# Optimization experiments

Hardware: AMD Instinct MI355X
Metric: run time of the kernel (lower is better)

Reference implementation:

```python
import jax, jax.numpy as jnp
import numpy as np

E = 1024   # embed_size
H = 16     # num_heads
D = E // H # head_dim
B, S = 4, 2048

def setup_inputs() -> dict:
    key = jax.random.key(0)
    ks = jax.random.split(key, 11)
    scale = 1.0 / np.sqrt(E)
    inp = {
        "Q": jax.random.normal(ks[0], (B, S, E), jnp.float32),
        "K": jax.random.normal(ks[1], (B, S, E), jnp.float32),
        "V": jax.random.normal(ks[2], (B, S, E), jnp.float32),
        "Wq": jax.random.uniform(ks[3], (E, E), jnp.float32, -scale, scale),
        "bq": jax.random.uniform(ks[4], (E,), jnp.float32, -scale, scale),
        "Wk": jax.random.uniform(ks[5], (E, E), jnp.float32, -scale, scale),
        "bk": jax.random.uniform(ks[6], (E,), jnp.float32, -scale, scale),
        "Wv": jax.random.uniform(ks[7], (E, E), jnp.float32, -scale, scale),
        "bv": jax.random.uniform(ks[8], (E,), jnp.float32, -scale, scale),
        "Wo": jax.random.uniform(ks[9], (E, E), jnp.float32, -scale, scale),
        "bo": jax.random.uniform(ks[10], (E,), jnp.float32, -scale, scale),
    }
    return inp

def reference(Q, K, V, Wq, bq, Wk, bk, Wv, bv, Wo, bo):
    b, sq, _ = Q.shape
    sk = K.shape[1]
    # Linear projections (torch Linear: x @ W.T + b), split into heads -> (b, H, s, D)
    q = (Q @ Wq.T + bq).reshape(b, sq, H, D).transpose(0, 2, 1, 3)
    k = (K @ Wk.T + bk).reshape(b, sk, H, D).transpose(0, 2, 1, 3)
    v = (V @ Wv.T + bv).reshape(b, sk, H, D).transpose(0, 2, 1, 3)
    scores = jnp.einsum('bhqd,bhkd->bhqk', q, k) / jnp.sqrt(jnp.float32(D))
    attn = jax.nn.softmax(scores, axis=-1)
    out = jnp.einsum('bhqk,bhkd->bhqd', attn, v)  # (b, H, sq, D)
    concat = out.transpose(0, 2, 1, 3).reshape(b, sq, E)
    return concat @ Wo.T + bo
```

## Files before the change

### kernel.cpp

```cpp
#include <hip/hip_runtime.h>
#include <hip/hip_bf16.h>

typedef unsigned short u16;
typedef unsigned int u32;
typedef __bf16 bf16x8 __attribute__((ext_vector_type(8)));
typedef float f32x4 __attribute__((ext_vector_type(4)));
typedef float f32x16 __attribute__((ext_vector_type(16)));
typedef unsigned int u32x2 __attribute__((ext_vector_type(2)));

constexpr int E_ = 1024, H_ = 16, D_ = 64, B_ = 4, S_ = 2048;
constexpr int GM = B_ * S_;
constexpr int GN = E_;
constexpr int GK = E_;

__device__ __forceinline__ u16 f2bf(float f) {
  union { float f; u32 u; } v; v.f = f;
  u32 r = v.u + 0x7fffu + ((v.u >> 16) & 1u);
  return (u16)(r >> 16);
}

__device__ __forceinline__ bf16x8 ld_bf16x8(const u16* p) {
  return *reinterpret_cast<const bf16x8*>(p);
}

__device__ __forceinline__ f32x4 mfma16(bf16x8 a, bf16x8 b, f32x4 c) {
  return __builtin_amdgcn_mfma_f32_16x16x32_bf16(a, b, c, 0, 0, 0);
}
__device__ __forceinline__ f32x16 mfma32(bf16x8 a, bf16x8 b, f32x16 c) {
  return __builtin_amdgcn_mfma_f32_32x32x16_bf16(a, b, c, 0, 0, 0);
}

__device__ __forceinline__ u32 cvtpk(float lo, float hi) {
  u32 r;
  asm("v_cvt_pk_bf16_f32 %0, %1, %2" : "=v"(r) : "v"(lo), "v"(hi));
  return r;
}

__device__ __forceinline__ void pl32swap(u32& a, u32& b) {
#if __has_builtin(__builtin_amdgcn_permlane32_swap)
  u32x2 r = __builtin_amdgcn_permlane32_swap(a, b, false, false);
  a = r.x; b = r.y;
#else
  asm volatile("v_permlane32_swap_b32 %0, %1" : "+v"(a), "+v"(b));
#endif
}

__device__ __forceinline__ float fexp2(float x) {
#if __has_builtin(__builtin_amdgcn_exp2f)
  return __builtin_amdgcn_exp2f(x);
#else
  return exp2f(x);
#endif
}

#define GLOAD_LDS16(gp, lp)                                                       \
  __builtin_amdgcn_global_load_lds(                                               \
      (const __attribute__((address_space(1))) u32*)(const void*)(gp),            \
      (__attribute__((address_space(3))) u32*)(void*)(lp), 16, 0, 0)

__global__ __launch_bounds__(256) void cvt7(
    const float4* __restrict__ s0, const float4* __restrict__ s1,
    const float4* __restrict__ s2, const float4* __restrict__ s3,
    const float4* __restrict__ s4, const float4* __restrict__ s5,
    const float4* __restrict__ s6,
    ushort4* __restrict__ d0, ushort4* __restrict__ d1,
    ushort4* __restrict__ d2, ushort4* __restrict__ d3,
    ushort4* __restrict__ d4, ushort4* __restrict__ d5,
    ushort4* __restrict__ d6) {
  long i = (long)blockIdx.x * 256 + threadIdx.x;
  const float4* s; ushort4* d; long j;
  if (i < 2097152L)      { s = s0; d = d0; j = i; }
  else if (i < 4194304L) { s = s1; d = d1; j = i - 2097152L; }
  else if (i < 6291456L) { s = s2; d = d2; j = i - 4194304L; }
  else if (i < 6553600L) { s = s3; d = d3; j = i - 6291456L; }
  else if (i < 6815744L) { s = s4; d = d4; j = i - 6553600L; }
  else if (i < 7077888L) { s = s5; d = d5; j = i - 6815744L; }
  else                   { s = s6; d = d6; j = i - 7077888L; }
  float4 v = s[j];
  ushort4 o;
  o.x = f2bf(v.x); o.y = f2bf(v.y); o.z = f2bf(v.z); o.w = f2bf(v.w);
  d[j] = o;
}

template <int MODE>
__global__ __launch_bounds__(256, 2) void gemm_bt(
    const u16* __restrict__ A, const u16* __restrict__ Bw,
    const float* __restrict__ bias, void* __restrict__ Cout, float scale) {
  __shared__ u16 As[128 * 32];
  __shared__ u16 Bs[128 * 32];
  const int tid = threadIdx.x;
  const int lane = tid & 63, w = tid >> 6;
  const int lr = lane & 15, lg = lane >> 4;
  const int bid = blockIdx.x;
  const int flat = (bid & 7) * 64 + (bid >> 3);
  const int bm = flat >> 3, bn = flat & 7;
  const int wm = (w >> 1) * 64, wn = (w & 1) * 64;

  f32x4 acc[4][4] = {};

  const int byte0 = (w * 2 + 0) * 1024 + lane * 16;
  const int byte1 = (w * 2 + 1) * 1024 + lane * 16;
  const int r0 = byte0 >> 6, c0 = (byte0 & 63) >> 1;
  const int r1 = byte1 >> 6, c1 = (byte1 & 63) >> 1;
  const u16* Arow0 = A + (size_t)(bm * 128 + r0) * GK + c0;
  const u16* Arow1 = A + (size_t)(bm * 128 + r1) * GK + c1;
  const u16* Brow0 = Bw + (size_t)(bn * 128 + r0) * GK + c0;
  const u16* Brow1 = Bw + (size_t)(bn * 128 + r1) * GK + c1;
  u16* As0 = &As[(w * 2 + 0) * 512];
  u16* As1 = &As[(w * 2 + 1) * 512];
  u16* Bs0 = &Bs[(w * 2 + 0) * 512];
  u16* Bs1 = &Bs[(w * 2 + 1) * 512];

  for (int kt = 0; kt < GK / 32; ++kt) {
    const int ko = kt * 32;
    GLOAD_LDS16(Arow0 + ko, As0);
    GLOAD_LDS16(Arow1 + ko, As1);
    GLOAD_LDS16(Brow0 + ko, Bs0);
    GLOAD_LDS16(Brow1 + ko, Bs1);
    __syncthreads();
    bf16x8 af[4], bf_[4];
#pragma unroll
    for (int mi = 0; mi < 4; ++mi)
      af[mi] = ld_bf16x8(&As[(wm + mi * 16 + lr) * 32 + lg * 8]);
#pragma unroll
    for (int ni = 0; ni < 4; ++ni)
      bf_[ni] = ld_bf16x8(&Bs[(wn + ni * 16 + lr) * 32 + lg * 8]);
#pragma unroll
    for (int mi = 0; mi < 4; ++mi)
#pragma unroll
      for (int ni = 0; ni < 4; ++ni)
        acc[mi][ni] = mfma16(af[mi], bf_[ni], acc[mi][ni]);
    __syncthreads();
  }

#pragma unroll
  for (int mi = 0; mi < 4; ++mi)
#pragma unroll
    for (int ni = 0; ni < 4; ++ni) {
      const int n = bn * 128 + wn + ni * 16 + lr;
      const float bv = bias[n];
#pragma unroll
      for (int r = 0; r < 4; ++r) {
        const int m = bm * 128 + wm + mi * 16 + lg * 4 + r;
        const float vv = (acc[mi][ni][r] + bv) * scale;
        if (MODE == 0) {
          const int b = m >> 11, s = m & 2047, h = n >> 6, d = n & 63;
          ((u16*)Cout)[(((size_t)(b * 16 + h) * 2048 + s) * 64) + d] = f2bf(vv);
        } else if (MODE == 1) {
          const int b = m >> 11, s = m & 2047, h = n >> 6, d = n & 63;
          ((u16*)Cout)[((size_t)(b * 16 + h) * 64 + d) * 2048 + s] = f2bf(vv);
        } else {
          ((float*)Cout)[(size_t)m * 1024 + n] = vv;
        }
      }
    }
}

__global__ __launch_bounds__(256, 2) void attn5(
    const u16* __restrict__ q, const u16* __restrict__ k,
    const u16* __restrict__ vT, u16* __restrict__ concat) {
  __shared__ u16 KT[2][64 * 64];
  __shared__ u16 VTl[2][64 * 64];
  const int tid = threadIdx.x, lane = tid & 63, w = tid >> 6;
  const int l31 = lane & 31, hi = lane >> 5;
  const int bid = blockIdx.x;
  const int flat = (bid & 7) * 64 + (bid >> 3);
  const int bh = flat >> 3, qt = flat & 7;
  const u16* qbp = q + (size_t)bh * S_ * D_;
  const char* kbase = (const char*)(k + (size_t)bh * S_ * D_);
  const char* vbase = (const char*)(vT + (size_t)bh * D_ * S_);
  const int q0 = qt * 256 + w * 64;

  bf16x8 qf[2][4];
#pragma unroll
  for (int qs = 0; qs < 2; ++qs)
#pragma unroll
    for (int kc = 0; kc < 4; ++kc)
      qf[qs][kc] =
          ld_bf16x8(&qbp[(size_t)(q0 + qs * 32 + l31) * 64 + kc * 16 + hi * 8]);

  f32x16 acc[2][2] = {};
  float l_[2] = {0.f, 0.f};

  const int srow = w * 8 + (lane >> 3);
  const int cswz = (((lane & 7) ^ (lane >> 3)) << 4);
  const char* gk0 = kbase + (size_t)srow * 128 + cswz;
  const char* gk1 = kbase + (size_t)(32 + srow) * 128 + cswz;
  const char* gv0 = vbase + (size_t)srow * (S_ * 2) + cswz;
  const char* gv1 = vbase + (size_t)(32 + srow) * (S_ * 2) + cswz;

  int col4[4];
#pragma unroll
  for (int c = 0; c < 4; ++c)
    col4[c] = (((c * 32 + hi * 16) ^ ((lane & 7) << 4)) >> 1);
  const int rrow = l31 * 64;

#define STAGE(t, buf)                                                     \
  do {                                                                    \
    GLOAD_LDS16(gk0 + (size_t)(t) * 8192, &KT[buf][(0 * 4 + w) * 512]);   \
    GLOAD_LDS16(gk1 + (size_t)(t) * 8192, &KT[buf][(1 * 4 + w) * 512]);   \
    GLOAD_LDS16(gv0 + (size_t)(t) * 128, &VTl[buf][(0 * 4 + w) * 512]);   \
    GLOAD_LDS16(gv1 + (size_t)(t) * 128, &VTl[buf][(1 * 4 + w) * 512]);   \
  } while (0)

  STAGE(0, 0);
  asm volatile("s_waitcnt vmcnt(0)" ::: "memory");
  __syncthreads();

  for (int t = 0; t < S_ / 64; ++t) {
    const int cur = t & 1, nxt = cur ^ 1;
    if (t < S_ / 64 - 1) STAGE(t + 1, nxt);

    f32x16 sF[2][2] = {};
#pragma unroll
    for (int st = 0; st < 2; ++st)
#pragma unroll
      for (int kc = 0; kc < 4; ++kc) {
        bf16x8 kf = ld_bf16x8(&KT[cur][st * 2048 + rrow + col4[kc]]);
        sF[0][st] = mfma32(kf, qf[0][kc], sF[0][st]);
        sF[1][st] = mfma32(kf, qf[1][kc], sF[1][st]);
      }

    bf16x8 vt[2][4];
#pragma unroll
    for (int ks = 0; ks < 4; ++ks) {
      vt[0][ks] = ld_bf16x8(&VTl[cur][rrow + col4[ks]]);
      vt[1][ks] = ld_bf16x8(&VTl[cur][2048 + rrow + col4[ks]]);
    }

#pragma unroll
    for (int qs = 0; qs < 2; ++qs) {
      float s0 = 0.f, s1 = 0.f, s2 = 0.f, s3 = 0.f;
#pragma unroll
      for (int st = 0; st < 2; ++st)
#pragma unroll
        for (int e = 0; e < 16; e += 4) {
          const float p0 = fexp2(sF[qs][st][e + 0]);
          const float p1 = fexp2(sF[qs][st][e + 1]);
          const float p2 = fexp2(sF[qs][st][e + 2]);
          const float p3 = fexp2(sF[qs][st][e + 3]);
          sF[qs][st][e + 0] = p0; sF[qs][st][e + 1] = p1;
          sF[qs][st][e + 2] = p2; sF[qs][st][e + 3] = p3;
          s0 += p0; s1 += p1; s2 += p2; s3 += p3;
        }
      l_[qs] += (s0 + s1) + (s2 + s3);

#pragma unroll
      for (int ks = 0; ks < 4; ++ks) {
        const int st = ks >> 1, b = (ks & 1) * 8;
        u32 w0 = cvtpk(sF[qs][st][b + 0], sF[qs][st][b + 1]);
        u32 w1 = cvtpk(sF[qs][st][b + 2], sF[qs][st][b + 3]);
        u32 w2 = cvtpk(sF[qs][st][b + 4], sF[qs][st][b + 5]);
        u32 w3 = cvtpk(sF[qs][st][b + 6], sF[qs][st][b + 7]);
        pl32swap(w0, w2);
        pl32swap(w1, w3);
        union { u32 u[4]; bf16x8 v; } pa;
        pa.u[0] = w0; pa.u[1] = w1; pa.u[2] = w2; pa.u[3] = w3;
        acc[qs][0] = mfma32(vt[0][ks], pa.v, acc[qs][0]);
        acc[qs][1] = mfma32(vt[1][ks], pa.v, acc[qs][1]);
      }
    }

    asm volatile("s_waitcnt vmcnt(0)" ::: "memory");
    __syncthreads();
  }
#undef STAGE

  const int b = bh >> 4, h = bh & 15;
#pragma unroll
  for (int qs = 0; qs < 2; ++qs) {
    u32 la = __builtin_bit_cast(u32, l_[qs]), lb = la;
    pl32swap(la, lb);
    const float lt =
        __builtin_bit_cast(float, la) + __builtin_bit_cast(float, lb);
    const float inv = 1.f / lt;
    const int s = q0 + qs * 32 + l31;
    u16* crow = concat + ((size_t)(b * 2048 + s)) * 1024 + h * 64;
#pragma unroll
    for (int dt = 0; dt < 2; ++dt)
#pragma unroll
      for (int g = 0; g < 4; ++g) {
        ushort4 o;
        o.x = f2bf(acc[qs][dt][g * 4 + 0] * inv);
        o.y = f2bf(acc[qs][dt][g * 4 + 1] * inv);
        o.z = f2bf(acc[qs][dt][g * 4 + 2] * inv);
        o.w = f2bf(acc[qs][dt][g * 4 + 3] * inv);
        *(ushort4*)&crow[dt * 32 + g * 8 + hi * 4] = o;
      }
  }
}

extern "C" void kernel_launch(void* const* d_in, const int* in_sizes, int n_in,
                              void* d_out, int out_size, void* d_ws,
                              size_t ws_size, hipStream_t stream) {
  const float* Qf = (const float*)d_in[0];
  const float* Kf = (const float*)d_in[1];
  const float* Vf = (const float*)d_in[2];
  const float* Wq = (const float*)d_in[3];
  const float* bq = (const float*)d_in[4];
  const float* Wk = (const float*)d_in[5];
  const float* bk = (const float*)d_in[6];
  const float* Wv = (const float*)d_in[7];
  const float* bv = (const float*)d_in[8];
  const float* Wo = (const float*)d_in[9];
  const float* bo = (const float*)d_in[10];

  char* ws = (char*)d_ws;
  u16* Xq = (u16*)(ws);
  u16* Xk = Xq + 8388608;
  u16* Xv = Xk + 8388608;
  u16* Wqb = (u16*)(ws + (size_t)3 * 16777216);
  u16* Wkb = Wqb + 1048576;
  u16* Wvb = Wkb + 1048576;
  u16* Wob = Wvb + 1048576;
  u16* qb = (u16*)(ws + (size_t)3 * 16777216 + 8388608);
  u16* kb = qb + (size_t)GM * GN;
  u16* vTb = kb + (size_t)GM * GN;
  u16* concat = Xq;

  cvt7<<<28672, 256, 0, stream>>>(
      (const float4*)Qf, (const float4*)Kf, (const float4*)Vf,
      (const float4*)Wq, (const float4*)Wk, (const float4*)Wv,
      (const float4*)Wo, (ushort4*)Xq, (ushort4*)Xk, (ushort4*)Xv,
      (ushort4*)Wqb, (ushort4*)Wkb, (ushort4*)Wvb, (ushort4*)Wob);

  gemm_bt<0><<<512, 256, 0, stream>>>(Xq, Wqb, bq, qb, 0.18033688011112042f);
  gemm_bt<0><<<512, 256, 0, stream>>>(Xk, Wkb, bk, kb, 1.0f);
  gemm_bt<1><<<512, 256, 0, stream>>>(Xv, Wvb, bv, vTb, 1.0f);

  attn5<<<512, 256, 0, stream>>>(qb, kb, vTb, concat);

  gemm_bt<2><<<512, 256, 0, stream>>>(concat, Wob, bo, (void*)d_out, 1.0f);
}
```

Baseline: 209.8 us.

## Split attention KV range across two blocks and merge partial outputs

```diff
diff --git a/kernel.cpp b/kernel.cpp
--- a/kernel.cpp
+++ b/kernel.cpp
@@ -156,20 +156,23 @@
     }
 }
 
-__global__ __launch_bounds__(256, 2) void attn5(
+__global__ __launch_bounds__(256, 2) void attn_part(
     const u16* __restrict__ q, const u16* __restrict__ k,
-    const u16* __restrict__ vT, u16* __restrict__ concat) {
+    const u16* __restrict__ vT, float* __restrict__ Ppart,
+    float* __restrict__ lpart) {
   __shared__ u16 KT[2][64 * 64];
   __shared__ u16 VTl[2][64 * 64];
   const int tid = threadIdx.x, lane = tid & 63, w = tid >> 6;
   const int l31 = lane & 31, hi = lane >> 5;
   const int bid = blockIdx.x;
-  const int flat = (bid & 7) * 64 + (bid >> 3);
-  const int bh = flat >> 3, qt = flat & 7;
+  const int flat = (bid & 7) * 128 + (bid >> 3);
+  const int gq = flat >> 1, half = flat & 1;
+  const int bh = gq >> 3, qt = gq & 7;
   const u16* qbp = q + (size_t)bh * S_ * D_;
   const char* kbase = (const char*)(k + (size_t)bh * S_ * D_);
   const char* vbase = (const char*)(vT + (size_t)bh * D_ * S_);
   const int q0 = qt * 256 + w * 64;
+  const int t0 = half * 16;
 
   bf16x8 qf[2][4];
 #pragma unroll
@@ -203,13 +206,13 @@
     GLOAD_LDS16(gv1 + (size_t)(t) * 128, &VTl[buf][(1 * 4 + w) * 512]);   \
   } while (0)
 
-  STAGE(0, 0);
+  STAGE(t0, 0);
   asm volatile("s_waitcnt vmcnt(0)" ::: "memory");
   __syncthreads();
 
-  for (int t = 0; t < S_ / 64; ++t) {
-    const int cur = t & 1, nxt = cur ^ 1;
-    if (t < S_ / 64 - 1) STAGE(t + 1, nxt);
+  for (int tt = 0; tt < 16; ++tt) {
+    const int cur = tt & 1, nxt = cur ^ 1;
+    if (tt < 15) STAGE(t0 + tt + 1, nxt);
 
     f32x16 sF[2][2] = {};
 #pragma unroll
@@ -266,27 +269,56 @@
   }
 #undef STAGE
 
-  const int b = bh >> 4, h = bh & 15;
+  float* Pb = Ppart + (size_t)flat * 16384;
 #pragma unroll
   for (int qs = 0; qs < 2; ++qs) {
+    const int qlocal = w * 64 + qs * 32 + l31;
+    float* prow = Pb + qlocal * 64;
+#pragma unroll
+    for (int dt = 0; dt < 2; ++dt)
+#pragma unroll
+      for (int g = 0; g < 4; ++g) {
+        float4 o;
+        o.x = acc[qs][dt][g * 4 + 0];
+        o.y = acc[qs][dt][g * 4 + 1];
+        o.z = acc[qs][dt][g * 4 + 2];
+        o.w = acc[qs][dt][g * 4 + 3];
+        *(float4*)&prow[dt * 32 + g * 8 + hi * 4] = o;
+      }
     u32 la = __builtin_bit_cast(u32, l_[qs]), lb = la;
     pl32swap(la, lb);
     const float lt =
         __builtin_bit_cast(float, la) + __builtin_bit_cast(float, lb);
-    const float inv = 1.f / lt;
-    const int s = q0 + qs * 32 + l31;
-    u16* crow = concat + ((size_t)(b * 2048 + s)) * 1024 + h * 64;
-#pragma unroll
-    for (int dt = 0; dt < 2; ++dt)
-#pragma unroll
-      for (int g = 0; g < 4; ++g) {
-        ushort4 o;
-        o.x = f2bf(acc[qs][dt][g * 4 + 0] * inv);
-        o.y = f2bf(acc[qs][dt][g * 4 + 1] * inv);
-        o.z = f2bf(acc[qs][dt][g * 4 + 2] * inv);
-        o.w = f2bf(acc[qs][dt][g * 4 + 3] * inv);
-        *(ushort4*)&crow[dt * 32 + g * 8 + hi * 4] = o;
-      }
+    if (hi == 0) lpart[(size_t)flat * 256 + qlocal] = lt;
+  }
+}
+
+__global__ __launch_bounds__(256) void attn_merge(
+    const float* __restrict__ Ppart, const float* __restrict__ lpart,
+    u16* __restrict__ concat) {
+  const int bid = blockIdx.x;
+  const int gq = (bid & 7) * 64 + (bid >> 3);
+  const int bh = gq >> 3, qt = gq & 7;
+  const int b = bh >> 4, h = bh & 15;
+  const float* P0 = Ppart + ((size_t)gq * 2 + 0) * 16384;
+  const float* P1 = Ppart + ((size_t)gq * 2 + 1) * 16384;
+  const float* l0 = lpart + ((size_t)gq * 2 + 0) * 256;
+  const float* l1 = lpart + ((size_t)gq * 2 + 1) * 256;
+  const int t = threadIdx.x;
+#pragma unroll
+  for (int i = 0; i < 16; ++i) {
+    const int idx = i * 1024 + t * 4;
+    const int qq = idx >> 6, d = idx & 63;
+    const float inv = 1.f / (l0[qq] + l1[qq]);
+    const float4 a = *(const float4*)&P0[idx];
+    const float4 c = *(const float4*)&P1[idx];
+    ushort4 o;
+    o.x = f2bf((a.x + c.x) * inv);
+    o.y = f2bf((a.y + c.y) * inv);
+    o.z = f2bf((a.z + c.z) * inv);
+    o.w = f2bf((a.w + c.w) * inv);
+    const int s = qt * 256 + qq;
+    *(ushort4*)&concat[((size_t)(b * 2048 + s)) * 1024 + h * 64 + d] = o;
   }
 }
 
@@ -306,17 +338,20 @@
   const float* bo = (const float*)d_in[10];
 
   char* ws = (char*)d_ws;
-  u16* Xq = (u16*)(ws);
-  u16* Xk = Xq + 8388608;
-  u16* Xv = Xk + 8388608;
-  u16* Wqb = (u16*)(ws + (size_t)3 * 16777216);
+  constexpr size_t MB = 1048576;
+  u16* qb = (u16*)ws;
+  u16* kb = qb + (size_t)GM * GN;
+  u16* vTb = kb + (size_t)GM * GN;
+  u16* Wqb = (u16*)(ws + 48 * MB);
   u16* Wkb = Wqb + 1048576;
   u16* Wvb = Wkb + 1048576;
   u16* Wob = Wvb + 1048576;
-  u16* qb = (u16*)(ws + (size_t)3 * 16777216 + 8388608);
-  u16* kb = qb + (size_t)GM * GN;
-  u16* vTb = kb + (size_t)GM * GN;
-  u16* concat = Xq;
+  u16* Xq = (u16*)(ws + 56 * MB);
+  u16* Xk = Xq + 8388608;
+  u16* Xv = Xk + 8388608;
+  float* Ppart = (float*)(ws + 56 * MB);
+  float* lpart = (float*)(ws + 120 * MB);
+  u16* concat = qb;
 
   cvt7<<<28672, 256, 0, stream>>>(
       (const float4*)Qf, (const float4*)Kf, (const float4*)Vf,
@@ -328,7 +363,8 @@
   gemm_bt<0><<<512, 256, 0, stream>>>(Xk, Wkb, bk, kb, 1.0f);
   gemm_bt<1><<<512, 256, 0, stream>>>(Xv, Wvb, bv, vTb, 1.0f);
 
-  attn5<<<512, 256, 0, stream>>>(qb, kb, vTb, concat);
+  attn_part<<<1024, 256, 0, stream>>>(qb, kb, vTb, Ppart, lpart);
+  attn_merge<<<512, 256, 0, stream>>>(Ppart, lpart, concat);
 
   gemm_bt<2><<<512, 256, 0, stream>>>(concat, Wob, bo, (void*)d_out, 1.0f);
 }
```

Result: slower. 224.7 us (+7.1%).
